# Optimization experiments

Measured on AMD Instinct MI355X. Metric: run time of the kernel, lower is better.

The kernel has to match this reference:

```python
import jax, jax.numpy as jnp
import numpy as np

WK = 5        # fine_window_size
STRIDE = 4    # hardcoded in forward
PAD = WK // 2


def _gather_windows(feat, b, idx):
    # feat: [N, C, H, W]; b, idx: [M]. Replicates F.unfold(k=5, s=4, p=2)
    # followed by permute/reshape(n, l, W^2, c) and advanced indexing,
    # but only materializes the M selected windows (fused unfold+gather).
    N, C, H, W = feat.shape
    out_w = (W + 2 * PAD - WK) // STRIDE + 1
    fp = jnp.pad(feat, ((0, 0), (0, 0), (PAD, PAD), (PAD, PAD)))
    gy = idx // out_w
    gx = idx % out_w
    rows = gy[:, None] * STRIDE + jnp.arange(WK)   # [M, WK]
    cols = gx[:, None] * STRIDE + jnp.arange(WK)   # [M, WK]
    # advanced indices at axes 0,2,3 with slice at axis 1 -> [M, WK, WK, C]
    patch = fp[b[:, None, None], :, rows[:, :, None], cols[:, None, :]]
    # F.unfold flattens channel-major (C, kh, kw); the torch code then
    # reshapes that C*WK*WK axis as (WK*WK, C) -- an index-mixing reshape
    # we must replicate exactly.
    M = b.shape[0]
    patch = patch.transpose(0, 3, 1, 2).reshape(M, C * WK * WK)
    return patch.reshape(M, WK * WK, C)


def setup_inputs() -> dict:
    key = jax.random.key(0)
    k0, k1, kb, ki, kj = jax.random.split(key, 5)
    N, C, H, W = 4, 128, 240, 320
    L = (H // STRIDE) * (W // STRIDE)  # 4800 coarse positions
    M = 6000
    return {
        "feat_f0": jax.random.normal(k0, (N, C, H, W), dtype=jnp.float32),
        "feat_f1": jax.random.normal(k1, (N, C, H, W), dtype=jnp.float32),
        "hw0_f": jnp.array([H, W], dtype=jnp.int64),
        "hw0_c": jnp.array([H // STRIDE, W // STRIDE], dtype=jnp.int64),
        "b_ids": jax.random.randint(kb, (M,), 0, N, dtype=jnp.int64),
        "i_ids": jax.random.randint(ki, (M,), 0, L, dtype=jnp.int64),
        "j_ids": jax.random.randint(kj, (M,), 0, L, dtype=jnp.int64),
    }


def reference(feat_f0, feat_f1, hw0_f, hw0_c, b_ids, i_ids, j_ids):
    feat0 = _gather_windows(feat_f0, b_ids, i_ids)  # [M, W^2, C]
    feat1 = _gather_windows(feat_f1, b_ids, j_ids)  # [M, W^2, C]
    return feat0, feat1
```

## Files before the change

### kernel.cpp

```cpp
#include <hip/hip_runtime.h>


#define MPTS 6000
#define NCH  128
#define FH   240
#define FW   320
#define OUTW 80
#define MAPSZ (MPTS * NCH * 25)

__global__ __launch_bounds__(256) void fine_gather_kernel(
    const float* __restrict__ f0, const float* __restrict__ f1,
    const int* __restrict__ b_ids, const int* __restrict__ i_ids,
    const int* __restrict__ j_ids, float* __restrict__ out)
{
    const int total = 2 * MPTS * NCH * 5;
    int tid = blockIdx.x * 256 + threadIdx.x;
    if (tid >= total) return;

    int r   = tid % 5;
    int t1  = tid / 5;
    int c   = t1 % NCH;
    int t2  = t1 / NCH;
    int m   = t2 % MPTS;
    int map = t2 / MPTS;

    int b   = b_ids[m];
    int idx = map ? j_ids[m] : i_ids[m];
    const float* feat = map ? f1 : f0;

    int gy = idx / OUTW;
    int gx = idx - gy * OUTW;
    int row  = gy * 4 + r - 2;
    int col0 = gx * 4 - 2;

    bool vrow = (row >= 0) && (row < FH);
    const float* src = feat + (((long)(b * NCH + c) * FH + row) * FW + col0);

    long opos = (long)map * MAPSZ + ((long)(m * NCH + c) * 5 + r) * 5;

    float v[5];
#pragma unroll
    for (int k = 0; k < 5; k++) {
        int cc = col0 + k;
        bool ok = vrow && (cc >= 0) && (cc < FW);
        v[k] = ok ? src[k] : 0.0f;
    }
#pragma unroll
    for (int k = 0; k < 5; k++) out[opos + k] = v[k];
}

extern "C" void kernel_launch(void* const* d_in, const int* in_sizes, int n_in,
                              void* d_out, int out_size, void* d_ws, size_t ws_size,
                              hipStream_t stream) {
    const float* f0   = (const float*)d_in[0];
    const float* f1   = (const float*)d_in[1];
    const int* b_ids  = (const int*)d_in[4];
    const int* i_ids  = (const int*)d_in[5];
    const int* j_ids  = (const int*)d_in[6];
    float* out        = (float*)d_out;

    const int total  = 2 * MPTS * NCH * 5;
    const int blocks = (total + 255) / 256;
    fine_gather_kernel<<<blocks, 256, 0, stream>>>(f0, f1, b_ids, i_ids, j_ids, out);
}
```

Measured before the change: 479.0 us.

## Stage each window in LDS and write it out with float4 stores, one block per point

Launches one 320-thread block per selected point and map. Each thread loads window rows into shared memory, using 8-byte vector loads when the row and left column are in bounds. After a barrier, the block writes the contiguous 3200-float output slice with coalesced float4 stores instead of strided 5-float scalar stores. This adds a barrier and an LDS round trip per block, and it drops the right-edge column check, which the fixed stride geometry makes safe.

```diff
diff --git a/kernel.cpp b/kernel.cpp
--- a/kernel.cpp
+++ b/kernel.cpp
@@ -6,47 +6,65 @@
 #define FH   240
 #define FW   320
 #define OUTW 80
-#define MAPSZ (MPTS * NCH * 25)
+#define PTFLOATS (NCH * 25)
 
-__global__ __launch_bounds__(256) void fine_gather_kernel(
+typedef float f2 __attribute__((ext_vector_type(2)));
+
+__global__ __launch_bounds__(320) void fine_gather_kernel(
     const float* __restrict__ f0, const float* __restrict__ f1,
     const int* __restrict__ b_ids, const int* __restrict__ i_ids,
     const int* __restrict__ j_ids, float* __restrict__ out)
 {
-    const int total = 2 * MPTS * NCH * 5;
-    int tid = blockIdx.x * 256 + threadIdx.x;
-    if (tid >= total) return;
+    __shared__ __align__(16) float lds[PTFLOATS];
 
-    int r   = tid % 5;
-    int t1  = tid / 5;
-    int c   = t1 % NCH;
-    int t2  = t1 / NCH;
-    int m   = t2 % MPTS;
-    int map = t2 / MPTS;
+    const int blk = blockIdx.x;
+    const int map = blk >= MPTS;
+    const int m   = map ? blk - MPTS : blk;
+    const float* __restrict__ feat = map ? f1 : f0;
+    const int idx = map ? j_ids[m] : i_ids[m];
+    const int b   = b_ids[m];
 
-    int b   = b_ids[m];
-    int idx = map ? j_ids[m] : i_ids[m];
-    const float* feat = map ? f1 : f0;
+    const int gy = idx / OUTW;
+    const int gx = idx - gy * OUTW;
+    const int row0 = gy * 4 - 2;
+    const int col0 = gx * 4 - 2;
 
-    int gy = idx / OUTW;
-    int gx = idx - gy * OUTW;
-    int row  = gy * 4 + r - 2;
-    int col0 = gx * 4 - 2;
+    const int t = threadIdx.x;
 
-    bool vrow = (row >= 0) && (row < FH);
-    const float* src = feat + (((long)(b * NCH + c) * FH + row) * FW + col0);
+#pragma unroll
+    for (int it = 0; it < 2; it++) {
+        const int s = t + it * 320;
+        const int c = s / 5;
+        const int r = s - c * 5;
+        const int row = row0 + r;
+        const bool vrow = (row >= 0) & (row < FH);
+        const float* src = feat + (((long)(b * NCH + c) * FH + row) * FW + col0);
 
-    long opos = (long)map * MAPSZ + ((long)(m * NCH + c) * 5 + r) * 5;
+        float v[5];
+        if (vrow && (col0 >= 0)) {
+            const f2* p = (const f2*)src;
+            f2 a0 = p[0];
+            f2 a1 = p[1];
+            v[0] = a0.x; v[1] = a0.y; v[2] = a1.x; v[3] = a1.y;
+            v[4] = src[4];
+        } else {
+#pragma unroll
+            for (int k = 0; k < 5; k++) {
+                const int cc = col0 + k;
+                v[k] = (vrow && cc >= 0) ? src[k] : 0.0f;
+            }
+        }
+        const int base = s * 5;
+#pragma unroll
+        for (int k = 0; k < 5; k++) lds[base + k] = v[k];
+    }
 
-    float v[5];
-#pragma unroll
-    for (int k = 0; k < 5; k++) {
-        int cc = col0 + k;
-        bool ok = vrow && (cc >= 0) && (cc < FW);
-        v[k] = ok ? src[k] : 0.0f;
-    }
-#pragma unroll
-    for (int k = 0; k < 5; k++) out[opos + k] = v[k];
+    __syncthreads();
+
+    float4* __restrict__ dst = (float4*)(out + (long)blk * PTFLOATS);
+    const float4* sl = (const float4*)lds;
+    for (int i = t; i < PTFLOATS / 4; i += 320)
+        dst[i] = sl[i];
 }
 
 extern "C" void kernel_launch(void* const* d_in, const int* in_sizes, int n_in,
@@ -59,7 +77,5 @@
     const int* j_ids  = (const int*)d_in[6];
     float* out        = (float*)d_out;
 
-    const int total  = 2 * MPTS * NCH * 5;
-    const int blocks = (total + 255) / 256;
-    fine_gather_kernel<<<blocks, 256, 0, stream>>>(f0, f1, b_ids, i_ids, j_ids, out);
+    fine_gather_kernel<<<2 * MPTS, 320, 0, stream>>>(f0, f1, b_ids, i_ids, j_ids, out);
 }
```

Measured after the change: 438.2 us. 1.09x faster.
